# Performance work log

Measured on AMD Instinct MI355X. Metric: run time of the kernel, lower is better.

## Reference

```python
import jax, jax.numpy as jnp
import numpy as np

IN_FEATURES = 4096
OUT_FEATURES = 11008
BATCH = 16


def setup_inputs() -> dict:
    key = jax.random.key(0)
    k_x, k_w, k_s, k_b = jax.random.split(key, 4)
    x = jax.random.normal(k_x, (BATCH, IN_FEATURES), dtype=jnp.float32)
    # symmetric int8 weights stored as int32 for jax portability (values in [-127, 127])
    weight_int8 = jax.random.randint(k_w, (OUT_FEATURES, IN_FEATURES), -127, 128, dtype=jnp.int32)
    # per-output-channel scales, small positive values typical of int8 quantization
    weight_scale = jax.random.uniform(k_s, (OUT_FEATURES,), dtype=jnp.float32, minval=0.005, maxval=0.02)
    bias = jax.random.normal(k_b, (OUT_FEATURES,), dtype=jnp.float32)
    return {"x": x, "weight_int8": weight_int8, "weight_scale": weight_scale, "bias": bias}


def reference(x, weight_int8, weight_scale, bias):
    # Dequantize: w_dq[o, i] = int8[o, i] * scale[o]  -> fp32 [OUT, IN]
    w_dq = weight_int8.astype(x.dtype) * weight_scale[:, None]
    # F.linear: y = x @ w_dq.T + bias  -> [BATCH, OUT]
    return jnp.einsum("bi,oi->bo", x, w_dq) + bias
```

## Files before the change

kernel.cpp:

```cpp
#include <hip/hip_runtime.h>

#define IN_F   4096
#define OUT_F  11008
#define BATCH  16
#define TK     512
#define CO     16
#define BLOCK  256

__global__ __launch_bounds__(BLOCK) void qlin_kernel(
    const float* __restrict__ x,
    const int*   __restrict__ w,
    const float* __restrict__ scale,
    const float* __restrict__ bias,
    float* __restrict__ out)
{
    __shared__ float xs[BATCH][TK];

    const int tid = threadIdx.x;
    const int tx  = tid & 63;
    const int ty  = tid >> 6;
    const int o0  = blockIdx.x * CO + ty * 4;

    const int4* __restrict__ wbase = (const int4*)(w + (size_t)o0 * IN_F);

    float acc[64];
    #pragma unroll
    for (int i = 0; i < 64; ++i) acc[i] = 0.f;

    const float4* __restrict__ xg = (const float4*)x;

    for (int k0 = 0; k0 < IN_F; k0 += TK) {
        #pragma unroll
        for (int j = 0; j < (BATCH * TK / 4) / BLOCK; ++j) {
            int f  = tid + j * BLOCK;
            int b  = f >> 7;
            int kc = f & 127;
            float4 v = xg[(size_t)b * (IN_F / 4) + (k0 >> 2) + kc];
            *(float4*)&xs[b][kc * 4] = v;
        }
        __syncthreads();

        #pragma unroll
        for (int it = 0; it < TK / 256; ++it) {
            const int kl  = it * 256 + tx * 4;
            const int kg4 = (k0 >> 2) + it * 64 + tx;

            int4 w0 = wbase[kg4];
            int4 w1 = wbase[kg4 + 1 * (IN_F / 4)];
            int4 w2 = wbase[kg4 + 2 * (IN_F / 4)];
            int4 w3 = wbase[kg4 + 3 * (IN_F / 4)];

            float wf[4][4];
            wf[0][0] = (float)w0.x; wf[0][1] = (float)w0.y; wf[0][2] = (float)w0.z; wf[0][3] = (float)w0.w;
            wf[1][0] = (float)w1.x; wf[1][1] = (float)w1.y; wf[1][2] = (float)w1.z; wf[1][3] = (float)w1.w;
            wf[2][0] = (float)w2.x; wf[2][1] = (float)w2.y; wf[2][2] = (float)w2.z; wf[2][3] = (float)w2.w;
            wf[3][0] = (float)w3.x; wf[3][1] = (float)w3.y; wf[3][2] = (float)w3.z; wf[3][3] = (float)w3.w;

            #pragma unroll
            for (int bc = 0; bc < 4; ++bc) {
                float4 xv[4];
                #pragma unroll
                for (int bb = 0; bb < 4; ++bb)
                    xv[bb] = *(const float4*)&xs[bc * 4 + bb][kl];

                #pragma unroll
                for (int r = 0; r < 4; ++r)
                    #pragma unroll
                    for (int bb = 0; bb < 4; ++bb) {
                        float a = acc[r * 16 + bc * 4 + bb];
                        a += wf[r][0] * xv[bb].x;
                        a += wf[r][1] * xv[bb].y;
                        a += wf[r][2] * xv[bb].z;
                        a += wf[r][3] * xv[bb].w;
                        acc[r * 16 + bc * 4 + bb] = a;
                    }
            }
        }
        __syncthreads();
    }

    #pragma unroll
    for (int wd = 32; wd >= 1; wd >>= 1) {
        const bool upper = (tx & wd) != 0;
        #pragma unroll
        for (int i = 0; i < wd; ++i) {
            float lo = acc[i]      + __shfl_xor(acc[i],      wd);
            float hi = acc[i + wd] + __shfl_xor(acc[i + wd], wd);
            acc[i] = upper ? hi : lo;
        }
    }

    const int r_out = tx >> 4;
    const int b_out = tx & 15;
    const int o     = o0 + r_out;
    out[(size_t)b_out * OUT_F + o] = acc[0] * scale[o] + bias[o];
}

extern "C" void kernel_launch(void* const* d_in, const int* in_sizes, int n_in,
                              void* d_out, int out_size, void* d_ws, size_t ws_size,
                              hipStream_t stream) {
    const float* x     = (const float*)d_in[0];
    const int*   w     = (const int*)d_in[1];
    const float* scale = (const float*)d_in[2];
    const float* bias  = (const float*)d_in[3];
    float* out = (float*)d_out;

    dim3 grid(OUT_F / CO);
    dim3 block(BLOCK);
    qlin_kernel<<<grid, block, 0, stream>>>(x, w, scale, bias, out);
}
```

Measured before the change: 267.2 us.

## Split K across blocks with atomic accumulation, async LDS loads, nontemporal weights

```diff
diff --git a/kernel.cpp b/kernel.cpp
--- a/kernel.cpp
+++ b/kernel.cpp
@@ -6,12 +6,25 @@
 #define TK     512
 #define CO     16
 #define BLOCK  256
+#define SPLITK 4
+#define KCHUNK (IN_F / SPLITK)
+
+typedef int   i32x4 __attribute__((ext_vector_type(4)));
+
+__global__ __launch_bounds__(BLOCK) void init_out_kernel(
+    const float* __restrict__ bias, float* __restrict__ out)
+{
+    int idx = blockIdx.x * BLOCK + threadIdx.x;
+    if (idx < BATCH * OUT_F) {
+        int o = idx % OUT_F;
+        out[idx] = bias[o];
+    }
+}
 
 __global__ __launch_bounds__(BLOCK) void qlin_kernel(
     const float* __restrict__ x,
     const int*   __restrict__ w,
     const float* __restrict__ scale,
-    const float* __restrict__ bias,
     float* __restrict__ out)
 {
     __shared__ float xs[BATCH][TK];
@@ -20,41 +33,47 @@
     const int tx  = tid & 63;
     const int ty  = tid >> 6;
     const int o0  = blockIdx.x * CO + ty * 4;
+    const int kb  = blockIdx.y * KCHUNK;
 
-    const int4* __restrict__ wbase = (const int4*)(w + (size_t)o0 * IN_F);
+    const i32x4* __restrict__ wbase = (const i32x4*)(w + (size_t)o0 * IN_F);
 
     float acc[64];
     #pragma unroll
     for (int i = 0; i < 64; ++i) acc[i] = 0.f;
 
-    const float4* __restrict__ xg = (const float4*)x;
-
-    for (int k0 = 0; k0 < IN_F; k0 += TK) {
+    for (int k0 = kb; k0 < kb + KCHUNK; k0 += TK) {
         #pragma unroll
         for (int j = 0; j < (BATCH * TK / 4) / BLOCK; ++j) {
             int f  = tid + j * BLOCK;
             int b  = f >> 7;
             int kc = f & 127;
-            float4 v = xg[(size_t)b * (IN_F / 4) + (k0 >> 2) + kc];
-            *(float4*)&xs[b][kc * 4] = v;
+            const float* src = x + (size_t)b * IN_F + k0 + kc * 4;
+            void* dst = (char*)&xs[0][0] + (size_t)f * 16;
+            __builtin_amdgcn_global_load_lds(
+                (const __attribute__((address_space(1))) void*)src,
+                (__attribute__((address_space(3))) void*)dst,
+                16, 0, 0);
         }
         __syncthreads();
 
         #pragma unroll
         for (int it = 0; it < TK / 256; ++it) {
-            const int kl  = it * 256 + tx * 4;
-            const int kg4 = (k0 >> 2) + it * 64 + tx;
+            const int    kl  = it * 256 + tx * 4;
+            const size_t kg4 = (size_t)((k0 >> 2) + it * 64 + tx);
 
-            int4 w0 = wbase[kg4];
-            int4 w1 = wbase[kg4 + 1 * (IN_F / 4)];
-            int4 w2 = wbase[kg4 + 2 * (IN_F / 4)];
-            int4 w3 = wbase[kg4 + 3 * (IN_F / 4)];
+            i32x4 w0 = __builtin_nontemporal_load(wbase + kg4);
+            i32x4 w1 = __builtin_nontemporal_load(wbase + kg4 + 1 * (IN_F / 4));
+            i32x4 w2 = __builtin_nontemporal_load(wbase + kg4 + 2 * (IN_F / 4));
+            i32x4 w3 = __builtin_nontemporal_load(wbase + kg4 + 3 * (IN_F / 4));
 
             float wf[4][4];
-            wf[0][0] = (float)w0.x; wf[0][1] = (float)w0.y; wf[0][2] = (float)w0.z; wf[0][3] = (float)w0.w;
-            wf[1][0] = (float)w1.x; wf[1][1] = (float)w1.y; wf[1][2] = (float)w1.z; wf[1][3] = (float)w1.w;
-            wf[2][0] = (float)w2.x; wf[2][1] = (float)w2.y; wf[2][2] = (float)w2.z; wf[2][3] = (float)w2.w;
-            wf[3][0] = (float)w3.x; wf[3][1] = (float)w3.y; wf[3][2] = (float)w3.z; wf[3][3] = (float)w3.w;
+            #pragma unroll
+            for (int e = 0; e < 4; ++e) {
+                wf[0][e] = (float)w0[e];
+                wf[1][e] = (float)w1[e];
+                wf[2][e] = (float)w2[e];
+                wf[3][e] = (float)w3[e];
+            }
 
             #pragma unroll
             for (int bc = 0; bc < 4; ++bc) {
@@ -90,10 +109,9 @@
         }
     }
 
-    const int r_out = tx >> 4;
-    const int b_out = tx & 15;
-    const int o     = o0 + r_out;
-    out[(size_t)b_out * OUT_F + o] = acc[0] * scale[o] + bias[o];
+    const int o = o0 + (tx >> 4);
+    const int b = tx & 15;
+    atomicAdd(&out[(size_t)b * OUT_F + o], acc[0] * scale[o]);
 }
 
 extern "C" void kernel_launch(void* const* d_in, const int* in_sizes, int n_in,
@@ -105,7 +123,8 @@
     const float* bias  = (const float*)d_in[3];
     float* out = (float*)d_out;
 
-    dim3 grid(OUT_F / CO);
-    dim3 block(BLOCK);
-    qlin_kernel<<<grid, block, 0, stream>>>(x, w, scale, bias, out);
+    init_out_kernel<<<(BATCH * OUT_F + BLOCK - 1) / BLOCK, BLOCK, 0, stream>>>(bias, out);
+
+    dim3 grid(OUT_F / CO, SPLITK);
+    qlin_kernel<<<grid, dim3(BLOCK), 0, stream>>>(x, w, scale, out);
 }
```

New measurement: 259.3 us. 3.0% less time.
